# Kernel tuning notes

Hardware: AMD Instinct MI355X
Metric: run time of the kernel (lower is better)

## Reference

```python
import jax, jax.numpy as jnp
import numpy as np

N, D, T, ET, E = 100000, 128, 3, 4, 250000


def gru_cell(m, h, w_ih, w_hh, b_ih, b_hh):
    # torch.nn.GRUCell semantics
    gi = m @ w_ih.T + b_ih          # [N, 3D]
    gh = h @ w_hh.T + b_hh          # [N, 3D]
    i_r, i_z, i_n = jnp.split(gi, 3, axis=1)
    h_r, h_z, h_n = jnp.split(gh, 3, axis=1)
    r = jax.nn.sigmoid(i_r + h_r)
    z = jax.nn.sigmoid(i_z + h_z)
    n = jnp.tanh(i_n + r * h_n)
    return (1.0 - z) * n + z * h


def setup_inputs() -> dict:
    key = jax.random.key(0)
    ks = jax.random.split(key, 10)
    x = jax.random.normal(ks[0], (N, D), dtype=jnp.float32)
    edge_row = jax.random.randint(ks[1], (ET, E), 0, N, dtype=jnp.int32)
    edge_col = jax.random.randint(ks[2], (ET, E), 0, N, dtype=jnp.int32)
    edge_val = jnp.ones((ET, E), dtype=jnp.float32)
    xav = float(np.sqrt(6.0 / (D + D)))  # xavier_uniform per (D,D) slice
    weight = jax.random.uniform(ks[3], (T, ET, D, D), jnp.float32, -xav, xav)
    bias_w = jax.random.uniform(ks[4], (T, ET, D), jnp.float32, -0.01, 0.01)
    s = float(1.0 / np.sqrt(D))  # GRUCell default init range
    w_ih = jax.random.uniform(ks[5], (3 * D, D), jnp.float32, -s, s)
    w_hh = jax.random.uniform(ks[6], (3 * D, D), jnp.float32, -s, s)
    b_ih = jax.random.uniform(ks[7], (3 * D,), jnp.float32, -s, s)
    b_hh = jax.random.uniform(ks[8], (3 * D,), jnp.float32, -s, s)
    return {"x": x, "edge_row": edge_row, "edge_col": edge_col,
            "edge_val": edge_val, "weight": weight, "bias_w": bias_w,
            "w_ih": w_ih, "w_hh": w_hh, "b_ih": b_ih, "b_hh": b_hh}


def reference(x, edge_row, edge_col, edge_val, weight, bias_w, w_ih, w_hh, b_ih, b_hh):
    n_nodes = x.shape[0]
    h = x  # input_dim == out_channels, no zero-padding needed
    num_t = weight.shape[0]

    def agg_one(m_e, col_e, row_e, val_e):
        # sparse.mm: out[row] += val * m[col]
        msg = m_e[col_e] * val_e[:, None]                 # [E, D]
        return jax.ops.segment_sum(msg, row_e, num_segments=n_nodes)

    for t in range(num_t):
        # per-edge-type dense transform: [ET, N, D]
        m = jnp.einsum('nd,edf->enf', h, weight[t]) + bias_w[t][:, None, :]
        agg = jax.vmap(agg_one)(m, edge_col, edge_row, edge_val)  # [ET, N, D]
        m_sum = agg.sum(axis=0)                                    # [N, D]
        h = gru_cell(m_sum, h, w_ih, w_hh, b_ih, b_hh)
    return h
```

## Files before the change

### kernel.cpp

```cpp
#include <hip/hip_runtime.h>
#include <stdint.h>

#define NN  100000
#define DD  128
#define TT  3
#define ETT 4
#define EE  250000
#define NCH 49
#define GRUGRID 512

typedef float  f32x4  __attribute__((ext_vector_type(4)));
typedef __bf16 bf16x8 __attribute__((ext_vector_type(8)));

__device__ __forceinline__ float bf2f(uint32_t u){ u <<= 16; return __builtin_bit_cast(float, u); }
__device__ __forceinline__ uint32_t f2bf(float f){
  uint32_t u = __builtin_bit_cast(uint32_t, f);
  return (u + 0x7FFFu + ((u >> 16) & 1u)) >> 16;
}
__device__ __forceinline__ f32x4 mfma16(bf16x8 a, bf16x8 b, f32x4 c){
  return __builtin_amdgcn_mfma_f32_16x16x32_bf16(a, b, c, 0, 0, 0);
}

__global__ void k_count_m(const int* __restrict__ erow, const float* __restrict__ eval,
                          int* __restrict__ counts_m, float* __restrict__ degval){
  int idx = blockIdx.x * 256 + threadIdx.x;
  if (idx >= ETT * EE) return;
  int e = idx / EE;
  int row = erow[idx];
  atomicAdd(&counts_m[row], 1);
  atomicAdd(&degval[e * NN + row], eval[idx]);
}

__global__ void k_blksum_m(const int* __restrict__ counts, int* __restrict__ bsum){
  const int b = blockIdx.x;
  const int* p = counts + b * 2048;
  int lim = NN - b * 2048; if (lim > 2048) lim = 2048;
  const int t = threadIdx.x;
  int s = 0;
  #pragma unroll
  for (int i = 0; i < 8; ++i){
    int idx = i * 256 + t;
    if (idx < lim) s += p[idx];
  }
  #pragma unroll
  for (int d = 32; d; d >>= 1) s += __shfl_down(s, d);
  __shared__ int wsum[4];
  if ((t & 63) == 0) wsum[t >> 6] = s;
  __syncthreads();
  if (t == 0) bsum[b] = wsum[0] + wsum[1] + wsum[2] + wsum[3];
}

__global__ void k_scanp_m(const int* __restrict__ bsum, int* __restrict__ bexc,
                          int* __restrict__ offm){
  const int l = threadIdx.x;
  int v = (l < NCH) ? bsum[l] : 0;
  int x = v;
  #pragma unroll
  for (int d = 1; d < 64; d <<= 1){ int y = __shfl_up(x, d); if (l >= d) x += y; }
  if (l < NCH) bexc[l] = x - v;
  if (l == NCH - 1) offm[NN] = x;
}

__global__ void k_apply_m(const int* __restrict__ counts, const int* __restrict__ bexc,
                          int* __restrict__ offm){
  const int b = blockIdx.x;
  const int* p = counts + b * 2048;
  int* off = offm + b * 2048;
  int lim = NN - b * 2048; if (lim > 2048) lim = 2048;
  const int t = threadIdx.x, l = t & 63, wid = t >> 6;
  __shared__ int wt[4];
  int v[8], s = 0;
  #pragma unroll
  for (int i = 0; i < 8; ++i){
    int idx = t * 8 + i;
    v[i] = (idx < lim) ? p[idx] : 0; s += v[i];
  }
  int x = s;
  #pragma unroll
  for (int d = 1; d < 64; d <<= 1){ int y = __shfl_up(x, d); if (l >= d) x += y; }
  if (l == 63) wt[wid] = x;
  __syncthreads();
  int wexc = 0;
  #pragma unroll
  for (int k = 0; k < 4; ++k) if (k < wid) wexc += wt[k];
  int te = bexc[b] + wexc + (x - s);
  #pragma unroll
  for (int i = 0; i < 8; ++i){
    int idx = t * 8 + i;
    if (idx < lim) off[idx] = te;
    te += v[i];
  }
}

__global__ void k_fill_m(const int* __restrict__ erow, const int* __restrict__ ecol,
                         const float* __restrict__ eval, const int* __restrict__ offm,
                         int* __restrict__ cursor, uint2* __restrict__ sedge_m){
  int idx = blockIdx.x * 256 + threadIdx.x;
  if (idx >= ETT * EE) return;
  int e = idx / EE;
  int row = erow[idx];
  int pos = atomicAdd(&cursor[row], 1);
  int o = offm[row] + pos;
  sedge_m[o] = make_uint2((uint32_t)ecol[idx] | ((uint32_t)e << 20),
                          __builtin_bit_cast(uint32_t, eval[idx]));
}

__global__ void k_conv_x(const float* __restrict__ x, uint16_t* __restrict__ hbf){
  int idx = blockIdx.x * 256 + threadIdx.x;
  const float4* xp = (const float4*)x;
  float4 a = xp[idx * 2], b = xp[idx * 2 + 1];
  uint32_t p0 = f2bf(a.x) | (f2bf(a.y) << 16);
  uint32_t p1 = f2bf(a.z) | (f2bf(a.w) << 16);
  uint32_t p2 = f2bf(b.x) | (f2bf(b.y) << 16);
  uint32_t p3 = f2bf(b.z) | (f2bf(b.w) << 16);
  ((uint4*)hbf)[idx] = make_uint4(p0, p1, p2, p3);
}

__global__ void k_conv_w(const float* __restrict__ weight, const float* __restrict__ wih,
                         const float* __restrict__ whh, const float* __restrict__ bih,
                         const float* __restrict__ bhh, uint16_t* __restrict__ wcatT,
                         uint16_t* __restrict__ wihb, uint16_t* __restrict__ whhb,
                         float* __restrict__ bcomb){
  int idx = blockIdx.x * 256 + threadIdx.x;
  if (idx < TT * 128 * 512){
    int t = idx / 65536; int rem = idx - t * 65536;
    int f = rem >> 9; int u = rem & 511;
    int e = u >> 7; int d = u & 127;
    wcatT[idx] = (uint16_t)f2bf(weight[(((t * 4 + e) * 128 + d) << 7) + f]);
  }
  if (idx < 384 * 128){
    wihb[idx] = (uint16_t)f2bf(wih[idx]);
    whhb[idx] = (uint16_t)f2bf(whh[idx]);
  }
  if (idx < 256) bcomb[idx] = bih[idx] + bhh[idx];
}

#define PROC(ev, hv, vk) { \
  const float f0 = bf2f(hv.x & 0xffffu), f1 = bf2f(hv.x >> 16); \
  const float f2 = bf2f(hv.y & 0xffffu), f3 = bf2f(hv.y >> 16); \
  const int et = (int)(ev.x >> 20); \
  const float vs0 = (et == 0) ? vk : 0.f; \
  const float vs1 = (et == 1) ? vk : 0.f; \
  const float vs2 = (et == 2) ? vk : 0.f; \
  const float vs3 = (et == 3) ? vk : 0.f; \
  acc[0][0] += vs0*f0; acc[0][1] += vs0*f1; acc[0][2] += vs0*f2; acc[0][3] += vs0*f3; \
  acc[1][0] += vs1*f0; acc[1][1] += vs1*f1; acc[1][2] += vs1*f2; acc[1][3] += vs1*f3; \
  acc[2][0] += vs2*f0; acc[2][1] += vs2*f1; acc[2][2] += vs2*f2; acc[2][3] += vs2*f3; \
  acc[3][0] += vs3*f0; acc[3][1] += vs3*f1; acc[3][2] += vs3*f2; acc[3][3] += vs3*f3; \
}

__global__ __launch_bounds__(1024, 8) void k_agg_gemm(
    const uint16_t* __restrict__ hbf, const int* __restrict__ offm,
    const uint2* __restrict__ sedge_m, const float* __restrict__ degval,
    const float* __restrict__ bias_w, const uint16_t* __restrict__ wcatT_t,
    int tstep, uint16_t* __restrict__ m_out)
{
  __shared__ uint16_t aggT[32 * 512];
  const int tid = threadIdx.x;
  const int node0 = blockIdx.x * 32;

  {
    const int nl = tid >> 5, q = tid & 31;
    const int n = node0 + nl;
    float acc[4][4];
    #pragma unroll
    for (int e = 0; e < 4; ++e)
      #pragma unroll
      for (int d = 0; d < 4; ++d) acc[e][d] = 0.f;

    const int s  = offm[n];
    const int en = offm[n + 1];
    #pragma unroll 1
    for (int i = s; i < en; i += 4){
      const int last = en - 1;
      const int i1 = (i + 1 < last) ? i + 1 : last;
      const int i2 = (i + 2 < last) ? i + 2 : last;
      const int i3 = (i + 3 < last) ? i + 3 : last;
      const uint2 e0 = sedge_m[i],  e1 = sedge_m[i1];
      const uint2 e2 = sedge_m[i2], e3 = sedge_m[i3];
      const float v0 = __builtin_bit_cast(float, e0.y);
      const float v1 = (i + 1 <= last) ? __builtin_bit_cast(float, e1.y) : 0.f;
      const float v2 = (i + 2 <= last) ? __builtin_bit_cast(float, e2.y) : 0.f;
      const float v3 = (i + 3 <= last) ? __builtin_bit_cast(float, e3.y) : 0.f;
      const uint2 h0 = *(const uint2*)(hbf + (size_t)(e0.x & 0xFFFFFu) * DD + q * 4);
      const uint2 h1 = *(const uint2*)(hbf + (size_t)(e1.x & 0xFFFFFu) * DD + q * 4);
      const uint2 h2 = *(const uint2*)(hbf + (size_t)(e2.x & 0xFFFFFu) * DD + q * 4);
      const uint2 h3 = *(const uint2*)(hbf + (size_t)(e3.x & 0xFFFFFu) * DD + q * 4);
      PROC(e0, h0, v0); PROC(e1, h1, v1); PROC(e2, h2, v2); PROC(e3, h3, v3);
    }

    #pragma unroll
    for (int e = 0; e < ETT; ++e){
      const int c  = e * 16 + (q >> 1);
      const int cs = c ^ (nl & 7);
      uint32_t p0 = f2bf(acc[e][0]) | (f2bf(acc[e][1]) << 16);
      uint32_t p1 = f2bf(acc[e][2]) | (f2bf(acc[e][3]) << 16);
      *(uint2*)&aggT[nl * 512 + cs * 8 + (q & 1) * 4] = make_uint2(p0, p1);
    }
  }
  __syncthreads();

  const int lane = tid & 63, w = tid >> 6;
  const int rlo = lane & 15, kg = lane >> 4;
  const int rt = w & 1, fc = w >> 1;
  const int rowA = rt * 16 + rlo;
  f32x4 C = f32x4{0.f, 0.f, 0.f, 0.f};

  #pragma unroll
  for (int ks = 0; ks < 16; ++ks){
    const int cs = (ks * 4 + kg) ^ (rowA & 7);
    bf16x8 a = __builtin_bit_cast(bf16x8, *(const uint4*)&aggT[rowA * 512 + cs * 8]);
    bf16x8 b = __builtin_bit_cast(bf16x8,
        *(const uint4*)(wcatT_t + (size_t)(fc * 16 + rlo) * 512 + ks * 32 + kg * 8));
    C = mfma16(a, b, C);
  }

  const float* bwt = bias_w + tstep * (ETT * DD);
  const int f = fc * 16 + rlo;
  const float b0 = bwt[f], b1 = bwt[128 + f], b2 = bwt[256 + f], b3 = bwt[384 + f];
  #pragma unroll
  for (int r = 0; r < 4; ++r){
    const int n2 = node0 + rt * 16 + kg * 4 + r;
    const float bias = degval[n2] * b0 + degval[NN + n2] * b1
                     + degval[2 * NN + n2] * b2 + degval[3 * NN + n2] * b3;
    m_out[(size_t)n2 * DD + f] = (uint16_t)f2bf(C[r] + bias);
  }
}

__global__ __launch_bounds__(512, 2) void k_gru(
    const uint16_t* __restrict__ m_sum, const uint16_t* __restrict__ hsrc,
    uint16_t* __restrict__ hdst, const float* __restrict__ h_old,
    float* __restrict__ h_new, const uint16_t* __restrict__ wihb,
    const uint16_t* __restrict__ whhb, const float* __restrict__ bcomb,
    const float* __restrict__ b_ih, const float* __restrict__ b_hh)
{
  __shared__ uint4 mt[2][512];
  __shared__ uint4 ht[2][512];
  const int tid = threadIdx.x;
  const int lane = tid & 63, w = tid >> 6;
  const int rlo = lane & 15, kg = lane >> 4;

  bf16x8 wa[3][4], wb[3][4];
  #pragma unroll
  for (int g = 0; g < 3; ++g){
    const int j = g * 128 + w * 16 + rlo;
    #pragma unroll
    for (int ks = 0; ks < 4; ++ks){
      wa[g][ks] = __builtin_bit_cast(bf16x8, *(const uint4*)(wihb + j * 128 + ks * 32 + kg * 8));
      wb[g][ks] = __builtin_bit_cast(bf16x8, *(const uint4*)(whhb + j * 128 + ks * 32 + kg * 8));
    }
  }
  const int d0 = w * 16 + kg * 4;
  const f32x4 brz = *(const f32x4*)(bcomb + d0);
  const f32x4 bzz = *(const f32x4*)(bcomb + 128 + d0);
  const f32x4 bin = *(const f32x4*)(b_ih + 256 + d0);
  const f32x4 bhn = *(const f32x4*)(b_hh + 256 + d0);

  const int sn  = tid >> 4;
  const int scs = tid & 15;
  const int sc  = scs ^ (sn & 7);

  const int NT = NN / 32;
  int tile = blockIdx.x;
  {
    const size_t base = ((size_t)(tile * 32 + sn)) * DD + sc * 8;
    mt[0][sn * 16 + scs] = *(const uint4*)(m_sum + base);
    ht[0][sn * 16 + scs] = *(const uint4*)(hsrc + base);
  }
  __syncthreads();

  int buf = 0;
  #pragma unroll 1
  for (; tile < NT; tile += GRUGRID){
    const int ntile = tile + GRUGRID;
    const bool have = ntile < NT;
    uint4 mv, hv;
    if (have){
      const size_t nbase = ((size_t)(ntile * 32 + sn)) * DD + sc * 8;
      mv = *(const uint4*)(m_sum + nbase);
      hv = *(const uint4*)(hsrc + nbase);
    }

    f32x4 acc[3][2][2];
    #pragma unroll
    for (int g = 0; g < 3; ++g)
      #pragma unroll
      for (int m = 0; m < 2; ++m)
        #pragma unroll
        for (int ns = 0; ns < 2; ++ns) acc[g][m][ns] = f32x4{0.f,0.f,0.f,0.f};

    #pragma unroll
    for (int ks = 0; ks < 4; ++ks){
      #pragma unroll
      for (int ns = 0; ns < 2; ++ns){
        const int node = ns * 16 + rlo;
        const int cs = (ks * 4 + kg) ^ (node & 7);
        const bf16x8 bm = __builtin_bit_cast(bf16x8, mt[buf][node * 16 + cs]);
        const bf16x8 bh = __builtin_bit_cast(bf16x8, ht[buf][node * 16 + cs]);
        #pragma unroll
        for (int g = 0; g < 3; ++g){
          acc[g][0][ns] = mfma16(wa[g][ks], bm, acc[g][0][ns]);
          acc[g][1][ns] = mfma16(wb[g][ks], bh, acc[g][1][ns]);
        }
      }
    }

    #pragma unroll
    for (int ns = 0; ns < 2; ++ns){
      const int node = tile * 32 + ns * 16 + rlo;
      const f32x4 ho = *(const f32x4*)(h_old + (size_t)node * DD + d0);
      float hvv[4];
      #pragma unroll
      for (int r = 0; r < 4; ++r){
        const float rg = 1.f / (1.f + __expf(-(acc[0][0][ns][r] + acc[0][1][ns][r] + brz[r])));
        const float zg = 1.f / (1.f + __expf(-(acc[1][0][ns][r] + acc[1][1][ns][r] + bzz[r])));
        const float xa = (acc[2][0][ns][r] + bin[r]) + rg * (acc[2][1][ns][r] + bhn[r]);
        const float ng = 1.f - 2.f / (__expf(2.f * xa) + 1.f);
        hvv[r] = (1.f - zg) * ng + zg * ho[r];
      }
      *(f32x4*)(h_new + (size_t)node * DD + d0) = f32x4{hvv[0], hvv[1], hvv[2], hvv[3]};
      uint32_t p0 = f2bf(hvv[0]) | (f2bf(hvv[1]) << 16);
      uint32_t p1 = f2bf(hvv[2]) | (f2bf(hvv[3]) << 16);
      *(uint2*)(hdst + (size_t)node * DD + d0) = make_uint2(p0, p1);
    }

    if (have){
      mt[buf ^ 1][sn * 16 + scs] = mv;
      ht[buf ^ 1][sn * 16 + scs] = hv;
    }
    __syncthreads();
    buf ^= 1;
  }
}

extern "C" void kernel_launch(void* const* d_in, const int* in_sizes, int n_in,
                              void* d_out, int out_size, void* d_ws, size_t ws_size,
                              hipStream_t stream) {
  const float* x      = (const float*)d_in[0];
  const int*   erow   = (const int*)d_in[1];
  const int*   ecol   = (const int*)d_in[2];
  const float* eval   = (const float*)d_in[3];
  const float* weight = (const float*)d_in[4];
  const float* bias_w = (const float*)d_in[5];
  const float* wih    = (const float*)d_in[6];
  const float* whh    = (const float*)d_in[7];
  const float* bih    = (const float*)d_in[8];
  const float* bhh    = (const float*)d_in[9];
  float* out = (float*)d_out;
  char* ws = (char*)d_ws;

  size_t o = 0;
  auto alloc = [&](size_t bytes)->char*{ char* p = ws + o; o += (bytes + 255) & ~(size_t)255; return p; };
  int*      counts_m = (int*)     alloc((size_t)NN * 4);
  int*      cursor_m = (int*)     alloc((size_t)NN * 4);
  float*    degval   = (float*)   alloc((size_t)ETT * NN * 4);
  int*      offm     = (int*)     alloc((size_t)(NN + 1) * 4);
  int*      bsum     = (int*)     alloc((size_t)NCH * 4);
  int*      bexc     = (int*)     alloc((size_t)NCH * 4);
  uint2*    sedge_m  = (uint2*)   alloc((size_t)ETT * EE * 8);
  float*    hf       = (float*)   alloc((size_t)NN * DD * 4);
  uint16_t* hbf0     = (uint16_t*)alloc((size_t)NN * DD * 2);
  uint16_t* hbf1     = (uint16_t*)alloc((size_t)NN * DD * 2);
  uint16_t* msum     = (uint16_t*)alloc((size_t)NN * DD * 2);
  uint16_t* wcatT    = (uint16_t*)alloc((size_t)TT * 128 * 512 * 2);
  uint16_t* wihb     = (uint16_t*)alloc((size_t)384 * 128 * 2);
  uint16_t* whhb     = (uint16_t*)alloc((size_t)384 * 128 * 2);
  float*    bcomb    = (float*)   alloc((size_t)256 * 4);
  (void)ws_size; (void)in_sizes; (void)n_in; (void)out_size;

  const size_t zspan = (size_t)((char*)degval - (char*)counts_m) + (size_t)ETT * NN * 4;
  hipMemsetAsync(counts_m, 0, zspan, stream);

  k_count_m<<<(ETT * EE + 255) / 256, 256, 0, stream>>>(erow, eval, counts_m, degval);
  k_blksum_m<<<NCH, 256, 0, stream>>>(counts_m, bsum);
  k_scanp_m<<<1, 64, 0, stream>>>(bsum, bexc, offm);
  k_apply_m<<<NCH, 256, 0, stream>>>(counts_m, bexc, offm);
  k_fill_m<<<(ETT * EE + 255) / 256, 256, 0, stream>>>(erow, ecol, eval, offm, cursor_m, sedge_m);
  k_conv_x<<<(NN * DD / 8) / 256, 256, 0, stream>>>(x, hbf0);
  k_conv_w<<<(TT * 128 * 512 + 255) / 256, 256, 0, stream>>>(weight, wih, whh, bih, bhh,
                                                             wcatT, wihb, whhb, bcomb);

  uint16_t* hsrc = hbf0;
  uint16_t* hdst = hbf1;
  for (int t = 0; t < TT; ++t){
    k_agg_gemm<<<NN / 32, 1024, 0, stream>>>(hsrc, offm, sedge_m, degval,
                                             bias_w, wcatT + (size_t)t * 65536, t, msum);
    const float* hold = (t == 0) ? x : hf;
    float* hnew = (t == TT - 1) ? out : hf;
    k_gru<<<GRUGRID, 512, 0, stream>>>(msum, hsrc, hdst, hold, hnew,
                                       wihb, whhb, bcomb, bih, bhh);
    uint16_t* tmp = hsrc; hsrc = hdst; hdst = tmp;
  }
}
```

Baseline: 780.3 us.

## Spread block edges across warps with LDS atomic scatter aggregation

Aggregation no longer gives each node one half-wave looping over its own edges. Each block now stages a chunk of its contiguous edge range into shared memory, and every half-wave takes edges round-robin, accumulating into a shared fp32 buffer with LDS atomic adds. To make this possible, the edge type and local row are packed into the column word. This is meant to remove load imbalance from uneven node degrees. In exchange it adds LDS atomic traffic and a larger shared-memory footprint (fp32 agg plus an edge buffer), which may reduce the number of resident blocks.

```diff
diff --git a/kernel.cpp b/kernel.cpp
--- a/kernel.cpp
+++ b/kernel.cpp
@@ -8,6 +8,7 @@
 #define EE  250000
 #define NCH 49
 #define GRUGRID 512
+#define ECHUNK 1024
 
 typedef float  f32x4  __attribute__((ext_vector_type(4)));
 typedef __bf16 bf16x8 __attribute__((ext_vector_type(8)));
@@ -101,7 +102,7 @@
   int row = erow[idx];
   int pos = atomicAdd(&cursor[row], 1);
   int o = offm[row] + pos;
-  sedge_m[o] = make_uint2((uint32_t)ecol[idx] | ((uint32_t)e << 20),
+  sedge_m[o] = make_uint2((uint32_t)ecol[idx] | ((uint32_t)e << 17) | (((uint32_t)row & 31u) << 19),
                           __builtin_bit_cast(uint32_t, eval[idx]));
 }
 
@@ -135,67 +136,87 @@
   if (idx < 256) bcomb[idx] = bih[idx] + bhh[idx];
 }
 
-#define PROC(ev, hv, vk) { \
-  const float f0 = bf2f(hv.x & 0xffffu), f1 = bf2f(hv.x >> 16); \
-  const float f2 = bf2f(hv.y & 0xffffu), f3 = bf2f(hv.y >> 16); \
-  const int et = (int)(ev.x >> 20); \
-  const float vs0 = (et == 0) ? vk : 0.f; \
-  const float vs1 = (et == 1) ? vk : 0.f; \
-  const float vs2 = (et == 2) ? vk : 0.f; \
-  const float vs3 = (et == 3) ? vk : 0.f; \
-  acc[0][0] += vs0*f0; acc[0][1] += vs0*f1; acc[0][2] += vs0*f2; acc[0][3] += vs0*f3; \
-  acc[1][0] += vs1*f0; acc[1][1] += vs1*f1; acc[1][2] += vs1*f2; acc[1][3] += vs1*f3; \
-  acc[2][0] += vs2*f0; acc[2][1] += vs2*f1; acc[2][2] += vs2*f2; acc[2][3] += vs2*f3; \
-  acc[3][0] += vs3*f0; acc[3][1] += vs3*f1; acc[3][2] += vs3*f2; acc[3][3] += vs3*f3; \
-}
-
 __global__ __launch_bounds__(1024, 8) void k_agg_gemm(
     const uint16_t* __restrict__ hbf, const int* __restrict__ offm,
     const uint2* __restrict__ sedge_m, const float* __restrict__ degval,
     const float* __restrict__ bias_w, const uint16_t* __restrict__ wcatT_t,
     int tstep, uint16_t* __restrict__ m_out)
 {
-  __shared__ uint16_t aggT[32 * 512];
+  __shared__ float agg[32 * 512];
+  __shared__ uint2 lds_e[ECHUNK];
   const int tid = threadIdx.x;
   const int node0 = blockIdx.x * 32;
 
   {
-    const int nl = tid >> 5, q = tid & 31;
-    const int n = node0 + nl;
-    float acc[4][4];
-    #pragma unroll
-    for (int e = 0; e < 4; ++e)
-      #pragma unroll
-      for (int d = 0; d < 4; ++d) acc[e][d] = 0.f;
-
-    const int s  = offm[n];
-    const int en = offm[n + 1];
+    f32x4 z = {0.f, 0.f, 0.f, 0.f};
+    #pragma unroll
+    for (int i = 0; i < 4; ++i) *(f32x4*)&agg[tid * 16 + i * 4] = z;
+  }
+  const int s  = offm[node0];
+  const int en = offm[node0 + 32];
+  __syncthreads();
+
+  const int es = tid >> 5, q = tid & 31;
+  #pragma unroll 1
+  for (int cb = s; cb < en; cb += ECHUNK){
+    const int cnt = min(en - cb, ECHUNK);
+    if (tid < cnt) lds_e[tid] = sedge_m[cb + tid];
+    __syncthreads();
+
     #pragma unroll 1
-    for (int i = s; i < en; i += 4){
-      const int last = en - 1;
-      const int i1 = (i + 1 < last) ? i + 1 : last;
-      const int i2 = (i + 2 < last) ? i + 2 : last;
-      const int i3 = (i + 3 < last) ? i + 3 : last;
-      const uint2 e0 = sedge_m[i],  e1 = sedge_m[i1];
-      const uint2 e2 = sedge_m[i2], e3 = sedge_m[i3];
-      const float v0 = __builtin_bit_cast(float, e0.y);
-      const float v1 = (i + 1 <= last) ? __builtin_bit_cast(float, e1.y) : 0.f;
-      const float v2 = (i + 2 <= last) ? __builtin_bit_cast(float, e2.y) : 0.f;
-      const float v3 = (i + 3 <= last) ? __builtin_bit_cast(float, e3.y) : 0.f;
-      const uint2 h0 = *(const uint2*)(hbf + (size_t)(e0.x & 0xFFFFFu) * DD + q * 4);
-      const uint2 h1 = *(const uint2*)(hbf + (size_t)(e1.x & 0xFFFFFu) * DD + q * 4);
-      const uint2 h2 = *(const uint2*)(hbf + (size_t)(e2.x & 0xFFFFFu) * DD + q * 4);
-      const uint2 h3 = *(const uint2*)(hbf + (size_t)(e3.x & 0xFFFFFu) * DD + q * 4);
-      PROC(e0, h0, v0); PROC(e1, h1, v1); PROC(e2, h2, v2); PROC(e3, h3, v3);
-    }
-
-    #pragma unroll
-    for (int e = 0; e < ETT; ++e){
-      const int c  = e * 16 + (q >> 1);
+    for (int k0 = es; k0 < cnt; k0 += 128){
+      uint2 ed[4]; uint2 hh[4]; float vv[4];
+      #pragma unroll
+      for (int i = 0; i < 4; ++i){
+        const int k = k0 + 32 * i;
+        const int kc = (k < cnt) ? k : (cnt - 1);
+        ed[i] = lds_e[kc];
+        vv[i] = (k < cnt) ? __builtin_bit_cast(float, ed[i].y) : 0.f;
+      }
+      #pragma unroll
+      for (int i = 0; i < 4; ++i){
+        const uint32_t col = ed[i].x & 0x1FFFFu;
+        hh[i] = *(const uint2*)(hbf + (size_t)col * DD + q * 4);
+      }
+      #pragma unroll
+      for (int i = 0; i < 4; ++i){
+        const uint32_t et   = (ed[i].x >> 17) & 3u;
+        const uint32_t lrow = (ed[i].x >> 19) & 31u;
+        float* base = &agg[lrow * 512 + et * 128 + q];
+        const float v = vv[i];
+        atomicAdd(base,      v * bf2f(hh[i].x & 0xffffu));
+        atomicAdd(base + 32, v * bf2f(hh[i].x >> 16));
+        atomicAdd(base + 64, v * bf2f(hh[i].y & 0xffffu));
+        atomicAdd(base + 96, v * bf2f(hh[i].y >> 16));
+      }
+    }
+    __syncthreads();
+  }
+
+  uint16_t* aggT = (uint16_t*)agg;
+  {
+    const int nl = tid >> 5, cc = tid & 31;
+    uint4 pend[2];
+    #pragma unroll
+    for (int t2 = 0; t2 < 2; ++t2){
+      const int c = cc * 2 + t2;
+      const int et = c >> 4, c8 = c & 15;
+      const float* b = &agg[nl * 512 + et * 128 + c8 * 2];
+      const float2 v0 = *(const float2*)(b);
+      const float2 v1 = *(const float2*)(b + 32);
+      const float2 v2 = *(const float2*)(b + 64);
+      const float2 v3 = *(const float2*)(b + 96);
+      pend[t2].x = f2bf(v0.x) | (f2bf(v1.x) << 16);
+      pend[t2].y = f2bf(v2.x) | (f2bf(v3.x) << 16);
+      pend[t2].z = f2bf(v0.y) | (f2bf(v1.y) << 16);
+      pend[t2].w = f2bf(v2.y) | (f2bf(v3.y) << 16);
+    }
+    __syncthreads();
+    #pragma unroll
+    for (int t2 = 0; t2 < 2; ++t2){
+      const int c = cc * 2 + t2;
       const int cs = c ^ (nl & 7);
-      uint32_t p0 = f2bf(acc[e][0]) | (f2bf(acc[e][1]) << 16);
-      uint32_t p1 = f2bf(acc[e][2]) | (f2bf(acc[e][3]) << 16);
-      *(uint2*)&aggT[nl * 512 + cs * 8 + (q & 1) * 4] = make_uint2(p0, p1);
+      *(uint4*)&aggT[nl * 512 + cs * 8] = pend[t2];
     }
   }
   __syncthreads();
```

After: 3.069 ms. +293.3%, slower.
